# Performance work log

Measured on AMD Instinct MI355X. Metric: run time of the kernel, lower is better.

Reference implementation:

```python
import jax, jax.numpy as jnp
import numpy as np

H = 1024   # hidden_dim
C = 56     # numchars
T = 64     # total_timesteps


def setup_inputs() -> dict:
    key = jax.random.key(0)
    ks = jax.random.split(key, 20)

    def p(k, shape, fan_in):
        # torch default Linear/LSTM init: U(-1/sqrt(fan), 1/sqrt(fan))
        return jax.random.uniform(k, shape, jnp.float32, -1.0, 1.0) / np.float32(np.sqrt(fan_in))

    return {
        "input_sentence": jax.random.normal(ks[0], (T, C), jnp.float32),
        # ErrorUnit.W per layer (top-layer ErrorUnit is never run)
        "W0_w": p(ks[1], (H, C), C), "W0_b": p(ks[2], (H,), C),
        "W1_w": p(ks[3], (H, H), H), "W1_b": p(ks[4], (H,), H),
        "W2_w": p(ks[5], (H, H), H), "W2_b": p(ks[6], (H,), H),
        # LSTM input weights; h0=c0=0 every call so W_hh is inert; b = b_ih + b_hh
        "Wih1": p(ks[7], (4 * H, 2 * H), H), "b1": p(ks[8], (4 * H,), H),
        "Wih2": p(ks[9], (4 * H, 2 * H), H), "b2": p(ks[10], (4 * H,), H),
        "Wih3": p(ks[11], (4 * H, H), H), "b3": p(ks[12], (4 * H,), H),
        # StateUnit.V (reconstruction) per layer >= 1; layer0's V is never used
        "V1_w": p(ks[13], (C, H), H), "V1_b": p(ks[14], (C,), H),
        "V2_w": p(ks[15], (H, H), H), "V2_b": p(ks[16], (H,), H),
        "V3_w": p(ks[17], (H, H), H), "V3_b": p(ks[18], (H,), H),
        "iternumber": 500,
    }


def _lstm_out(x, Wih, b):
    # nn.LSTM(seq=1, batch=1) with zero initial state: f-gate dead, h = o*tanh(i*g)
    z = Wih @ x + b
    i, _, g, o = jnp.split(z, 4)
    return jax.nn.sigmoid(o) * jnp.tanh(jax.nn.sigmoid(i) * jnp.tanh(g))


def reference(input_sentence, W0_w, W0_b, W1_w, W1_b, W2_w, W2_b,
              Wih1, b1, Wih2, b2, Wih3, b3,
              V1_w, V1_b, V2_w, V2_b, V3_w, V3_b, iternumber):
    lam = 1e-4 if iternumber <= 1000 else 1e-2  # lambda1 / lambda2 branch
    h, c = W0_w.shape

    def step(carry, x_t):
        # TD1, TD2: previous-timestep TD errors (fed to LSTM inputs)
        # recon1..3: previous-timestep reconstructions from the layer above
        TD1, TD2, recon1, recon2, recon3, loss = carry
        # layer 0: state is clamped to the input char
        nTD0 = x_t - recon1                        # [C]
        BU0 = W0_w @ nTD0 + W0_b                   # [H]
        loss = loss + jnp.sum(jnp.abs(nTD0))       # * lam**0
        # layer 1
        s1 = _lstm_out(jnp.concatenate([BU0, TD1]), Wih1, b1)
        nrecon1 = V1_w @ s1 + V1_b                 # [C]
        nTD1 = s1 - recon2
        BU1 = W1_w @ nTD1 + W1_b
        loss = loss + jnp.sum(jnp.abs(nTD1)) * lam
        # layer 2
        s2 = _lstm_out(jnp.concatenate([BU1, TD2]), Wih2, b2)
        nrecon2 = V2_w @ s2 + V2_b
        nTD2 = s2 - recon3
        BU2 = W2_w @ nTD2 + W2_b
        loss = loss + jnp.sum(jnp.abs(nTD2)) * (lam ** 2)
        # layer 3 (top): ErrorUnit never runs, its TD_err stays zero -> zero loss term
        s3 = _lstm_out(BU2, Wih3, b3)
        nrecon3 = V3_w @ s3 + V3_b
        return (nTD1, nTD2, nrecon1, nrecon2, nrecon3, loss), None

    z = lambda n: jnp.zeros((n,), jnp.float32)
    init = (z(h), z(h), z(c), z(h), z(h), jnp.float32(0.0))
    carry, _ = jax.lax.scan(step, init, input_sentence)
    return carry[-1]
```

## Files before the change

### kernel.cpp

```cpp
#include <hip/hip_runtime.h>

#define CC 56
#define TT 64
#define GRID 1024
#define NT 256
#define NFLAG 64
#define SS 32
#define FB (GRID * SS)
#define AGENT __HIP_MEMORY_SCOPE_AGENT

#define OFF_FWS   147456
#define OFF_W1BF  262144
#define OFF_W2BF  2359296
#define OFF_PRIV  4456448
#define PRIVB     32768

#define PM2  0
#define PM3  3072
#define PW1R 6144
#define PW2R 9216
#define PV2  12288
#define PV3  13312
#define PV1  14336
#define PA0  15360

#define FS1   0
#define FS2   1024
#define FS3   2048
#define FTD1  3072
#define FTD2  5120
#define FRC1  7168

static __device__ __forceinline__ float wredsum(float v) {
#pragma unroll
  for (int m = 32; m; m >>= 1) v += __shfl_xor(v, m, 64);
  return v;
}
static __device__ __forceinline__ float sigm(float x) { return 1.f / (1.f + __expf(-x)); }
static __device__ __forceinline__ float ftanh(float x) {
  x = fminf(15.f, fmaxf(-15.f, x));
  float e = __expf(2.f * x);
  return (e - 1.f) / (e + 1.f);
}

static __device__ __forceinline__ float2 cld2(const float* p) {
  unsigned long long u = __hip_atomic_load((const unsigned long long*)p, __ATOMIC_RELAXED, AGENT);
  union { unsigned long long u; float2 f; } c; c.u = u; return c.f;
}
static __device__ __forceinline__ float4 cld4(const float* p) {
  float2 a = cld2(p), b = cld2(p + 2);
  return make_float4(a.x, a.y, b.x, b.y);
}
static __device__ __forceinline__ float cld1(const float* p) {
  return __uint_as_float(__hip_atomic_load((const unsigned int*)p, __ATOMIC_RELAXED, AGENT));
}
static __device__ __forceinline__ void cst1(float* p, float v) {
  __hip_atomic_store((unsigned int*)p, __float_as_uint(v), __ATOMIC_RELAXED, AGENT);
}
static __device__ __forceinline__ void cstu2(unsigned* p, unsigned a, unsigned b) {
  unsigned long long u = (unsigned long long)a | ((unsigned long long)b << 32);
  __hip_atomic_store((unsigned long long*)p, u, __ATOMIC_RELAXED, AGENT);
}
static __device__ __forceinline__ int ldi(const int* p) {
  return __hip_atomic_load(p, __ATOMIC_RELAXED, AGENT);
}
static __device__ __forceinline__ void sti(int* p, int v) {
  __hip_atomic_store(p, v, __ATOMIC_RELAXED, AGENT);
}

static __device__ __forceinline__ unsigned bfp(float lo, float hi) {
  unsigned a = __float_as_uint(lo), b = __float_as_uint(hi);
  a = (a + 0x7fffu + ((a >> 16) & 1u)) >> 16;
  b = (b + 0x7fffu + ((b >> 16) & 1u)) >> 16;
  return a | (b << 16);
}
static __device__ __forceinline__ float blo(unsigned u) { return __uint_as_float(u << 16); }
static __device__ __forceinline__ float bhi(unsigned u) { return __uint_as_float(u & 0xffff0000u); }
static __device__ __forceinline__ float bdot2(uint2 w, float4 v) {
  float r = blo(w.x) * v.x;
  r = fmaf(bhi(w.x), v.y, r);
  r = fmaf(blo(w.y), v.z, r);
  r = fmaf(bhi(w.y), v.w, r);
  return r;
}

static __device__ __forceinline__ void warr(int* iws, int g, int b) {
  __syncthreads();
  if (threadIdx.x == 0) sti(iws + SS * b, g);
}
static __device__ __forceinline__ void wwait(int* iws, int g, int b) {
  if (b == 0) {
    const int* p0 = iws + SS * threadIdx.x;
    for (;;) {
      int a0 = ldi(p0), a1 = ldi(p0 + SS * 256), a2 = ldi(p0 + SS * 512), a3 = ldi(p0 + SS * 768);
      if (a0 >= g && a1 >= g && a2 >= g && a3 >= g) break;
      __builtin_amdgcn_s_sleep(1);
    }
    __syncthreads();
    if (threadIdx.x < NFLAG) sti(iws + FB + SS * threadIdx.x, g);
  } else {
    if (threadIdx.x == 0)
      while (ldi(iws + FB + SS * (b & (NFLAG - 1))) < g) __builtin_amdgcn_s_sleep(1);
  }
  __asm__ __volatile__("" ::: "memory");
  __syncthreads();
}

static __device__ __forceinline__ float dotw(const float* a, const float* c, int lane) {
  const float4* a4 = (const float4*)a;
  const float4* c4 = (const float4*)c;
  float acc = 0.f;
#pragma unroll
  for (int j = 0; j < 4; ++j) {
    float4 x = a4[lane * 4 + j], y = c4[lane * 4 + j];
    acc = fmaf(x.x, y.x, fmaf(x.y, y.y, fmaf(x.z, y.z, fmaf(x.w, y.w, acc))));
  }
  return wredsum(acc);
}

__global__ void __launch_bounds__(NT, 4) predcells(
    const float* __restrict__ inp,
    const float* __restrict__ W0w, const float* __restrict__ W0b,
    const float* __restrict__ W1w, const float* __restrict__ W1b,
    const float* __restrict__ W2w, const float* __restrict__ W2b,
    const float* __restrict__ Wi1, const float* __restrict__ b1,
    const float* __restrict__ Wi2, const float* __restrict__ b2,
    const float* __restrict__ Wi3, const float* __restrict__ b3,
    const float* __restrict__ V1w, const float* __restrict__ V1b,
    const float* __restrict__ V2w, const float* __restrict__ V2b,
    const float* __restrict__ V3w, const float* __restrict__ V3b,
    const int* __restrict__ itn,
    float* __restrict__ out, char* ws)
{
  const int tid = threadIdx.x;
  const int lane = tid & 63;
  const int wv = tid >> 6;
  const int b = blockIdx.x;
  const bool hasV1 = (b < CC);

  int* iws = (int*)ws;
  float* fws = (float*)(ws + OFF_FWS);
  unsigned short* w1bf = (unsigned short*)(ws + OFF_W1BF);
  unsigned short* w2bf = (unsigned short*)(ws + OFF_W2BF);
  unsigned short* priv = (unsigned short*)(ws + OFF_PRIV + (size_t)b * PRIVB);

  __shared__ float arow[6][1024];
  __shared__ float psX[6][4], psP[3][4], psA[3];
  __shared__ float cs1[3], cs2[3], cs3[3];

  const int gofs = (wv == 0) ? 0 : ((wv == 1) ? 2048 : 3072);

  {
    float4 r1 = ((const float4*)(W1w + (size_t)b * 1024))[tid];
    cstu2((unsigned*)(w1bf + (size_t)b * 1024 + 4 * tid), bfp(r1.x, r1.y), bfp(r1.z, r1.w));
    float4 r2 = ((const float4*)(W2w + (size_t)b * 1024))[tid];
    cstu2((unsigned*)(w2bf + (size_t)b * 1024 + 4 * tid), bfp(r2.x, r2.y), bfp(r2.z, r2.w));
  }
  warr(iws, 1, b);

  const float lam = (itn[0] <= 1000) ? 1e-4f : 1e-2f;
  const float lam2 = lam * lam;
  const float v1b_b = hasV1 ? V1b[b] : 0.f;
  const float v2b_b = V2b[b];
  const float v3b_b = V3b[b];
  float l0 = 0.f, l1 = 0.f, l2 = 0.f;

  if (wv < 3) {
    float c1v = b1[b + gofs] + dotw(Wi1 + (size_t)(b + gofs) * 2048, W0b, lane);
    float c2v = b2[b + gofs] + dotw(Wi2 + (size_t)(b + gofs) * 2048, W1b, lane);
    float c3v = b3[b + gofs] + dotw(Wi3 + (size_t)(b + gofs) * 1024, W2b, lane);
    if (lane == 0) { cs1[wv] = c1v; cs2[wv] = c2v; cs3[wv] = c3v; }
    if (lane < CC) {
      const float* wr = Wi1 + (size_t)(b + gofs) * 2048;
      float acc = 0.f;
      for (int k = 0; k < 1024; ++k) acc = fmaf(wr[k], W0w[k * CC + lane], acc);
      ((float*)(priv + PA0))[wv * CC + lane] = acc;
    }
    {
      float4 x = ((const float4*)(Wi1 + (size_t)(b + gofs) * 2048 + 1024))[lane];
      ((uint2*)(priv + PW1R + wv * 1024))[lane] = make_uint2(bfp(x.x, x.y), bfp(x.z, x.w));
      float4 y = ((const float4*)(Wi2 + (size_t)(b + gofs) * 2048 + 1024))[lane];
      ((uint2*)(priv + PW2R + wv * 1024))[lane] = make_uint2(bfp(y.x, y.y), bfp(y.z, y.w));
    }
  } else {
#pragma unroll
    for (int j = 0; j < 4; ++j) {
      int i = lane * 4 + j;
      float4 a = ((const float4*)(V2w + (size_t)b * 1024))[i];
      ((uint2*)(priv + PV2))[i] = make_uint2(bfp(a.x, a.y), bfp(a.z, a.w));
      float4 c = ((const float4*)(V3w + (size_t)b * 1024))[i];
      ((uint2*)(priv + PV3))[i] = make_uint2(bfp(c.x, c.y), bfp(c.z, c.w));
      if (hasV1) {
        float4 d = ((const float4*)(V1w + (size_t)b * 1024))[i];
        ((uint2*)(priv + PV1))[i] = make_uint2(bfp(d.x, d.y), bfp(d.z, d.w));
      }
    }
  }
  __syncthreads();
  if (wv < 3) {
    float p = 0.f, ax = 0.f;
    if (lane < CC) {
      float xv = inp[lane];
      p = ((const float*)(priv + PA0))[wv * CC + lane] * xv;
      ax = fabsf(xv);
    }
    p = wredsum(p);
    ax = wredsum(ax);
    if (lane == 0) psA[wv] = p;
    if (b == 0 && wv == 0) l0 += ax;
  }
  __syncthreads();
  if (tid == 0) {
    float s1v = sigm(psA[2] + cs1[2]) * ftanh(sigm(psA[0] + cs1[0]) * ftanh(psA[1] + cs1[1]));
    cst1(fws + FS1 + b, s1v);
    cst1(fws + FTD1 + b, s1v);
    cst1(fws + FS3 + b, 0.f);
    cst1(fws + FTD2 + 1024 + b, 0.f);
  }
  wwait(iws, 1, b);

  {
#pragma unroll
    for (int w = 0; w < 3; ++w) {
      int go = (w == 0) ? 0 : ((w == 1) ? 2048 : 3072);
      ((float4*)arow[w])[tid]     = ((const float4*)(Wi2 + (size_t)(b + go) * 2048))[tid];
      ((float4*)arow[3 + w])[tid] = ((const float4*)(Wi3 + (size_t)(b + go) * 1024))[tid];
    }
    __syncthreads();
    float ac[12];
#pragma unroll
    for (int j = 0; j < 12; ++j) ac[j] = 0.f;
    const uint2* wsrc = (const uint2*)w1bf;
#pragma unroll 4
    for (int k = 0; k < 1024; ++k) {
      uint2 wp = wsrc[k * 256 + tid];
      float f0 = blo(wp.x), f1 = bhi(wp.x), f2 = blo(wp.y), f3 = bhi(wp.y);
      float ai = arow[0][k], ag = arow[1][k], ao = arow[2][k];
      ac[0] = fmaf(ai, f0, ac[0]); ac[1] = fmaf(ai, f1, ac[1]); ac[2] = fmaf(ai, f2, ac[2]); ac[3] = fmaf(ai, f3, ac[3]);
      ac[4] = fmaf(ag, f0, ac[4]); ac[5] = fmaf(ag, f1, ac[5]); ac[6] = fmaf(ag, f2, ac[6]); ac[7] = fmaf(ag, f3, ac[7]);
      ac[8] = fmaf(ao, f0, ac[8]); ac[9] = fmaf(ao, f1, ac[9]); ac[10] = fmaf(ao, f2, ac[10]); ac[11] = fmaf(ao, f3, ac[11]);
    }
#pragma unroll
    for (int w = 0; w < 3; ++w)
      ((uint2*)(priv + PM2 + w * 1024))[tid] =
          make_uint2(bfp(ac[w * 4 + 0], ac[w * 4 + 1]), bfp(ac[w * 4 + 2], ac[w * 4 + 3]));
#pragma unroll
    for (int j = 0; j < 12; ++j) ac[j] = 0.f;
    wsrc = (const uint2*)w2bf;
#pragma unroll 4
    for (int k = 0; k < 1024; ++k) {
      uint2 wp = wsrc[k * 256 + tid];
      float f0 = blo(wp.x), f1 = bhi(wp.x), f2 = blo(wp.y), f3 = bhi(wp.y);
      float ai = arow[3][k], ag = arow[4][k], ao = arow[5][k];
      ac[0] = fmaf(ai, f0, ac[0]); ac[1] = fmaf(ai, f1, ac[1]); ac[2] = fmaf(ai, f2, ac[2]); ac[3] = fmaf(ai, f3, ac[3]);
      ac[4] = fmaf(ag, f0, ac[4]); ac[5] = fmaf(ag, f1, ac[5]); ac[6] = fmaf(ag, f2, ac[6]); ac[7] = fmaf(ag, f3, ac[7]);
      ac[8] = fmaf(ao, f0, ac[8]); ac[9] = fmaf(ao, f1, ac[9]); ac[10] = fmaf(ao, f2, ac[10]); ac[11] = fmaf(ao, f3, ac[11]);
    }
#pragma unroll
    for (int w = 0; w < 3; ++w)
      ((uint2*)(priv + PM3 + w * 1024))[tid] =
          make_uint2(bfp(ac[w * 4 + 0], ac[w * 4 + 1]), bfp(ac[w * 4 + 2], ac[w * 4 + 3]));
  }
  warr(iws, 2, b);

  int g = 2;
  const uint2* pm2 = (const uint2*)(priv + PM2);
  const uint2* pm3 = (const uint2*)(priv + PM3);
  const uint2* pw1r = (const uint2*)(priv + PW1R);
  const uint2* pw2r = (const uint2*)(priv + PW2R);
  const uint2* pv2 = (const uint2*)(priv + PV2);
  const uint2* pv3 = (const uint2*)(priv + PV3);
  const uint2* pv1 = (const uint2*)(priv + PV1);
  const float* a0p = (const float*)(priv + PA0);

  for (int t = 0; t < TT; ++t) {
    const int par = t & 1;
    float* td1cur = fws + FTD1 + par * 1024;
    float* td1nxt = fws + FTD1 + (par ^ 1) * 1024;
    float* td2old = fws + FTD2 + (par ^ 1) * 1024;
    float* td2cur = fws + FTD2 + par * 1024;

    uint2 wm2[3]; wm2[0] = pm2[tid]; wm2[1] = pm2[256 + tid]; wm2[2] = pm2[512 + tid];
    uint2 wv3 = pv3[tid];
    uint2 wv1; if (hasV1) wv1 = pv1[tid];
    {
      float4 v = cld4(td2old + 4 * tid);
      uint2 wr0 = pw2r[tid], wr1 = pw2r[256 + tid], wr2 = pw2r[512 + tid];
      float p0 = wredsum(bdot2(wr0, v));
      float p1 = wredsum(bdot2(wr1, v));
      float p2 = wredsum(bdot2(wr2, v));
      if (lane == 0) { psP[0][wv] = p0; psP[1][wv] = p1; psP[2][wv] = p2; }
    }
    wwait(iws, g, b);
    {
      float4 vtd1 = cld4(td1cur + 4 * tid);
      float4 vs3  = cld4(fws + FS3 + 4 * tid);
      float p0 = wredsum(bdot2(wm2[0], vtd1));
      float p1 = wredsum(bdot2(wm2[1], vtd1));
      float p2 = wredsum(bdot2(wm2[2], vtd1));
      float p3 = wredsum(bdot2(wv3, vs3));
      if (lane == 0) { psX[0][wv] = p0; psX[1][wv] = p1; psX[2][wv] = p2; psX[3][wv] = p3; }
      if (hasV1) {
        float4 vs1 = cld4(fws + FS1 + 4 * tid);
        float pv = wredsum(bdot2(wv1, vs1));
        if (lane == 0) psX[4][wv] = pv;
      }
      if (b == 0) {
        float al = wredsum(fabsf(vtd1.x) + fabsf(vtd1.y) + fabsf(vtd1.z) + fabsf(vtd1.w));
        if (lane == 0) psX[5][wv] = al;
      }
      __syncthreads();
      if (tid == 0) {
        float zi = psX[0][0] + psX[0][1] + psX[0][2] + psX[0][3] + psP[0][0] + psP[0][1] + psP[0][2] + psP[0][3] + cs2[0];
        float zg = psX[1][0] + psX[1][1] + psX[1][2] + psX[1][3] + psP[1][0] + psP[1][1] + psP[1][2] + psP[1][3] + cs2[1];
        float zo = psX[2][0] + psX[2][1] + psX[2][2] + psX[2][3] + psP[2][0] + psP[2][1] + psP[2][2] + psP[2][3] + cs2[2];
        float s2v = sigm(zo) * ftanh(sigm(zi) * ftanh(zg));
        float rc3v = (t == 0) ? 0.f : (psX[3][0] + psX[3][1] + psX[3][2] + psX[3][3] + v3b_b);
        cst1(fws + FS2 + b, s2v);
        cst1(td2cur + b, s2v - rc3v);
        if (hasV1) cst1(fws + FRC1 + b, psX[4][0] + psX[4][1] + psX[4][2] + psX[4][3] + v1b_b);
        if (b == 0) l1 += psX[5][0] + psX[5][1] + psX[5][2] + psX[5][3];
      }
    }
    warr(iws, ++g, b);

    uint2 wm3[3]; wm3[0] = pm3[tid]; wm3[1] = pm3[256 + tid]; wm3[2] = pm3[512 + tid];
    uint2 wv2 = pv2[tid];
    {
      float4 v = cld4(td1cur + 4 * tid);
      uint2 wr0 = pw1r[tid], wr1 = pw1r[256 + tid], wr2 = pw1r[512 + tid];
      float p0 = wredsum(bdot2(wr0, v));
      float p1 = wredsum(bdot2(wr1, v));
      float p2 = wredsum(bdot2(wr2, v));
      if (lane == 0) { psP[0][wv] = p0; psP[1][wv] = p1; psP[2][wv] = p2; }
    }
    wwait(iws, g, b);
    {
      float4 vtd2 = cld4(td2cur + 4 * tid);
      float4 vs2  = cld4(fws + FS2 + 4 * tid);
      float p0 = wredsum(bdot2(wm3[0], vtd2));
      float p1 = wredsum(bdot2(wm3[1], vtd2));
      float p2 = wredsum(bdot2(wm3[2], vtd2));
      float p3 = wredsum(bdot2(wv2, vs2));
      if (lane == 0) { psX[0][wv] = p0; psX[1][wv] = p1; psX[2][wv] = p2; psX[3][wv] = p3; }
      if (b == 0) {
        float al = wredsum(fabsf(vtd2.x) + fabsf(vtd2.y) + fabsf(vtd2.z) + fabsf(vtd2.w));
        if (lane == 0) psX[5][wv] = al;
      }
      if (wv < 3) {
        const int tn = (t < TT - 1) ? (t + 1) : (TT - 1);
        float p = 0.f, ax = 0.f;
        if (lane < CC) {
          float xv = inp[tn * CC + lane];
          float rcv = cld1(fws + FRC1 + lane);
          float nd = xv - rcv;
          p = a0p[wv * CC + lane] * nd;
          ax = fabsf(nd);
        }
        p = wredsum(p);
        ax = wredsum(ax);
        if (lane == 0) psA[wv] = p;
        if (b == 0 && wv == 0 && t < TT - 1) l0 += ax;
      }
      __syncthreads();
      if (tid == 0) {
        float z3i = psX[0][0] + psX[0][1] + psX[0][2] + psX[0][3] + cs3[0];
        float z3g = psX[1][0] + psX[1][1] + psX[1][2] + psX[1][3] + cs3[1];
        float z3o = psX[2][0] + psX[2][1] + psX[2][2] + psX[2][3] + cs3[2];
        cst1(fws + FS3 + b, sigm(z3o) * ftanh(sigm(z3i) * ftanh(z3g)));
        float rc2v = psX[3][0] + psX[3][1] + psX[3][2] + psX[3][3] + v2b_b;
        float z1i = psA[0] + psP[0][0] + psP[0][1] + psP[0][2] + psP[0][3] + cs1[0];
        float z1g = psA[1] + psP[1][0] + psP[1][1] + psP[1][2] + psP[1][3] + cs1[1];
        float z1o = psA[2] + psP[2][0] + psP[2][1] + psP[2][2] + psP[2][3] + cs1[2];
        float s1n = sigm(z1o) * ftanh(sigm(z1i) * ftanh(z1g));
        cst1(fws + FS1 + b, s1n);
        cst1(td1nxt + b, s1n - rc2v);
        if (b == 0) l2 += psX[5][0] + psX[5][1] + psX[5][2] + psX[5][3];
      }
    }
    warr(iws, ++g, b);
  }

  if (b == 0 && tid == 0) out[0] = l0 + lam * l1 + lam2 * l2;
}

extern "C" void kernel_launch(void* const* d_in, const int* in_sizes, int n_in,
                              void* d_out, int out_size, void* d_ws, size_t ws_size,
                              hipStream_t stream) {
  const float* inp = (const float*)d_in[0];
  const float* W0w = (const float*)d_in[1];
  const float* W0b = (const float*)d_in[2];
  const float* W1w = (const float*)d_in[3];
  const float* W1b = (const float*)d_in[4];
  const float* W2w = (const float*)d_in[5];
  const float* W2b = (const float*)d_in[6];
  const float* Wi1 = (const float*)d_in[7];
  const float* b1  = (const float*)d_in[8];
  const float* Wi2 = (const float*)d_in[9];
  const float* b2  = (const float*)d_in[10];
  const float* Wi3 = (const float*)d_in[11];
  const float* b3  = (const float*)d_in[12];
  const float* V1w = (const float*)d_in[13];
  const float* V1b = (const float*)d_in[14];
  const float* V2w = (const float*)d_in[15];
  const float* V2b = (const float*)d_in[16];
  const float* V3w = (const float*)d_in[17];
  const float* V3b = (const float*)d_in[18];
  const int*   itn = (const int*)d_in[19];

  hipLaunchKernelGGL(predcells, dim3(GRID), dim3(NT), 0, stream,
                     inp, W0w, W0b, W1w, W1b, W2w, W2b,
                     Wi1, b1, Wi2, b2, Wi3, b3,
                     V1w, V1b, V2w, V2b, V3w, V3b, itn,
                     (float*)d_out, (char*)d_ws);
}
```

Baseline: 1.110 ms.

## Replace grid barriers with per-element tagged data polling in timestep loop

Removes the two grid-wide barriers per timestep. Each published value is now stored together with a generation tag as one 64-bit atomic, and consumers spin-poll the specific elements they need until the tags reach the expected generation. This turns a global all-to-all barrier into dataflow synchronisation, so blocks can proceed as soon as their inputs are ready. The costs are doubled workspace size, polling traffic on 1024 elements per read, and a guard counter that can silently break out with stale data.

```diff
diff --git a/kernel.cpp b/kernel.cpp
--- a/kernel.cpp
+++ b/kernel.cpp
@@ -24,12 +24,14 @@
 #define PV1  14336
 #define PA0  15360
 
-#define FS1   0
-#define FS2   1024
-#define FS3   2048
-#define FTD1  3072
-#define FTD2  5120
-#define FRC1  7168
+#define GS1   0
+#define GS2   2048
+#define GS3   4096
+#define GTD1  6144
+#define GTD2  10240
+#define GRC1  14336
+
+#define PGUARD (1 << 20)
 
 static __device__ __forceinline__ float wredsum(float v) {
 #pragma unroll
@@ -47,16 +49,6 @@
   unsigned long long u = __hip_atomic_load((const unsigned long long*)p, __ATOMIC_RELAXED, AGENT);
   union { unsigned long long u; float2 f; } c; c.u = u; return c.f;
 }
-static __device__ __forceinline__ float4 cld4(const float* p) {
-  float2 a = cld2(p), b = cld2(p + 2);
-  return make_float4(a.x, a.y, b.x, b.y);
-}
-static __device__ __forceinline__ float cld1(const float* p) {
-  return __uint_as_float(__hip_atomic_load((const unsigned int*)p, __ATOMIC_RELAXED, AGENT));
-}
-static __device__ __forceinline__ void cst1(float* p, float v) {
-  __hip_atomic_store((unsigned int*)p, __float_as_uint(v), __ATOMIC_RELAXED, AGENT);
-}
 static __device__ __forceinline__ void cstu2(unsigned* p, unsigned a, unsigned b) {
   unsigned long long u = (unsigned long long)a | ((unsigned long long)b << 32);
   __hip_atomic_store((unsigned long long*)p, u, __ATOMIC_RELAXED, AGENT);
@@ -66,6 +58,31 @@
 }
 static __device__ __forceinline__ void sti(int* p, int v) {
   __hip_atomic_store(p, v, __ATOMIC_RELAXED, AGENT);
+}
+
+static __device__ __forceinline__ int ptag(float2 v) { return (int)__float_as_uint(v.y); }
+static __device__ __forceinline__ void pub(float* base, int i, float v, int tag) {
+  cstu2((unsigned*)(base + 2 * i), __float_as_uint(v), (unsigned)tag);
+}
+static __device__ __forceinline__ float4 poll4(const float* base, int i0, int want) {
+  const float* p = base + 2 * i0;
+  float2 a, b, c, d; int gd = 0;
+  for (;;) {
+    a = cld2(p); b = cld2(p + 2); c = cld2(p + 4); d = cld2(p + 6);
+    if (ptag(a) >= want && ptag(b) >= want && ptag(c) >= want && ptag(d) >= want) break;
+    if (++gd > PGUARD) break;
+  }
+  return make_float4(a.x, b.x, c.x, d.x);
+}
+static __device__ __forceinline__ float poll1(const float* base, int i, int want) {
+  const float* p = base + 2 * i;
+  float2 a; int gd = 0;
+  for (;;) {
+    a = cld2(p);
+    if (ptag(a) >= want) break;
+    if (++gd > PGUARD) break;
+  }
+  return a.x;
 }
 
 static __device__ __forceinline__ unsigned bfp(float lo, float hi) {
@@ -82,6 +99,9 @@
   r = fmaf(blo(w.y), v.z, r);
   r = fmaf(bhi(w.y), v.w, r);
   return r;
+}
+static __device__ __forceinline__ float asum4(float4 v) {
+  return fabsf(v.x) + fabsf(v.y) + fabsf(v.z) + fabsf(v.w);
 }
 
 static __device__ __forceinline__ void warr(int* iws, int g, int b) {
@@ -212,10 +232,10 @@
   __syncthreads();
   if (tid == 0) {
     float s1v = sigm(psA[2] + cs1[2]) * ftanh(sigm(psA[0] + cs1[0]) * ftanh(psA[1] + cs1[1]));
-    cst1(fws + FS1 + b, s1v);
-    cst1(fws + FTD1 + b, s1v);
-    cst1(fws + FS3 + b, 0.f);
-    cst1(fws + FTD2 + 1024 + b, 0.f);
+    pub(fws + GS1, b, s1v, 1);
+    pub(fws + GTD1, b, s1v, 1);
+    pub(fws + GS3, b, 0.f, 1);
+    pub(fws + GTD2 + 2048, b, 0.f, 1);
   }
   wwait(iws, 1, b);
 
@@ -261,9 +281,7 @@
       ((uint2*)(priv + PM3 + w * 1024))[tid] =
           make_uint2(bfp(ac[w * 4 + 0], ac[w * 4 + 1]), bfp(ac[w * 4 + 2], ac[w * 4 + 3]));
   }
-  warr(iws, 2, b);
-
-  int g = 2;
+
   const uint2* pm2 = (const uint2*)(priv + PM2);
   const uint2* pm3 = (const uint2*)(priv + PM3);
   const uint2* pw1r = (const uint2*)(priv + PW1R);
@@ -275,38 +293,42 @@
 
   for (int t = 0; t < TT; ++t) {
     const int par = t & 1;
-    float* td1cur = fws + FTD1 + par * 1024;
-    float* td1nxt = fws + FTD1 + (par ^ 1) * 1024;
-    float* td2old = fws + FTD2 + (par ^ 1) * 1024;
-    float* td2cur = fws + FTD2 + par * 1024;
+    float* td1cur = fws + GTD1 + par * 2048;
+    float* td1nxt = fws + GTD1 + (par ^ 1) * 2048;
+    float* td2old = fws + GTD2 + (par ^ 1) * 2048;
+    float* td2cur = fws + GTD2 + par * 2048;
+    const int w_old = (t + 2) >> 1;
+    const int w_td1 = (t >> 1) + 1;
+    const int w_s   = t + 1;
+    const int w_cur = ((t + 2) >> 1) + (t & 1);
+    const int p_td  = (t & 1) ? ((t + 3) >> 1) : ((t >> 1) + 1);
 
     uint2 wm2[3]; wm2[0] = pm2[tid]; wm2[1] = pm2[256 + tid]; wm2[2] = pm2[512 + tid];
     uint2 wv3 = pv3[tid];
     uint2 wv1; if (hasV1) wv1 = pv1[tid];
     {
-      float4 v = cld4(td2old + 4 * tid);
+      float4 v = poll4(td2old, 4 * tid, w_old);
       uint2 wr0 = pw2r[tid], wr1 = pw2r[256 + tid], wr2 = pw2r[512 + tid];
       float p0 = wredsum(bdot2(wr0, v));
       float p1 = wredsum(bdot2(wr1, v));
       float p2 = wredsum(bdot2(wr2, v));
       if (lane == 0) { psP[0][wv] = p0; psP[1][wv] = p1; psP[2][wv] = p2; }
     }
-    wwait(iws, g, b);
+    float4 vtd1 = poll4(td1cur, 4 * tid, w_td1);
     {
-      float4 vtd1 = cld4(td1cur + 4 * tid);
-      float4 vs3  = cld4(fws + FS3 + 4 * tid);
+      float4 vs3 = poll4(fws + GS3, 4 * tid, w_s);
       float p0 = wredsum(bdot2(wm2[0], vtd1));
       float p1 = wredsum(bdot2(wm2[1], vtd1));
       float p2 = wredsum(bdot2(wm2[2], vtd1));
       float p3 = wredsum(bdot2(wv3, vs3));
       if (lane == 0) { psX[0][wv] = p0; psX[1][wv] = p1; psX[2][wv] = p2; psX[3][wv] = p3; }
       if (hasV1) {
-        float4 vs1 = cld4(fws + FS1 + 4 * tid);
+        float4 vs1 = poll4(fws + GS1, 4 * tid, w_s);
         float pv = wredsum(bdot2(wv1, vs1));
         if (lane == 0) psX[4][wv] = pv;
       }
       if (b == 0) {
-        float al = wredsum(fabsf(vtd1.x) + fabsf(vtd1.y) + fabsf(vtd1.z) + fabsf(vtd1.w));
+        float al = wredsum(asum4(vtd1));
         if (lane == 0) psX[5][wv] = al;
       }
       __syncthreads();
@@ -316,35 +338,33 @@
         float zo = psX[2][0] + psX[2][1] + psX[2][2] + psX[2][3] + psP[2][0] + psP[2][1] + psP[2][2] + psP[2][3] + cs2[2];
         float s2v = sigm(zo) * ftanh(sigm(zi) * ftanh(zg));
         float rc3v = (t == 0) ? 0.f : (psX[3][0] + psX[3][1] + psX[3][2] + psX[3][3] + v3b_b);
-        cst1(fws + FS2 + b, s2v);
-        cst1(td2cur + b, s2v - rc3v);
-        if (hasV1) cst1(fws + FRC1 + b, psX[4][0] + psX[4][1] + psX[4][2] + psX[4][3] + v1b_b);
+        pub(fws + GS2, b, s2v, w_s);
+        pub(td2cur, b, s2v - rc3v, p_td);
+        if (hasV1) pub(fws + GRC1, b, psX[4][0] + psX[4][1] + psX[4][2] + psX[4][3] + v1b_b, w_s);
         if (b == 0) l1 += psX[5][0] + psX[5][1] + psX[5][2] + psX[5][3];
       }
-    }
-    warr(iws, ++g, b);
-
-    uint2 wm3[3]; wm3[0] = pm3[tid]; wm3[1] = pm3[256 + tid]; wm3[2] = pm3[512 + tid];
-    uint2 wv2 = pv2[tid];
+      __syncthreads();
+    }
+
     {
-      float4 v = cld4(td1cur + 4 * tid);
       uint2 wr0 = pw1r[tid], wr1 = pw1r[256 + tid], wr2 = pw1r[512 + tid];
-      float p0 = wredsum(bdot2(wr0, v));
-      float p1 = wredsum(bdot2(wr1, v));
-      float p2 = wredsum(bdot2(wr2, v));
+      float p0 = wredsum(bdot2(wr0, vtd1));
+      float p1 = wredsum(bdot2(wr1, vtd1));
+      float p2 = wredsum(bdot2(wr2, vtd1));
       if (lane == 0) { psP[0][wv] = p0; psP[1][wv] = p1; psP[2][wv] = p2; }
     }
-    wwait(iws, g, b);
     {
-      float4 vtd2 = cld4(td2cur + 4 * tid);
-      float4 vs2  = cld4(fws + FS2 + 4 * tid);
+      uint2 wm3[3]; wm3[0] = pm3[tid]; wm3[1] = pm3[256 + tid]; wm3[2] = pm3[512 + tid];
+      uint2 wv2 = pv2[tid];
+      float4 vtd2 = poll4(td2cur, 4 * tid, w_cur);
+      float4 vs2  = poll4(fws + GS2, 4 * tid, w_s);
       float p0 = wredsum(bdot2(wm3[0], vtd2));
       float p1 = wredsum(bdot2(wm3[1], vtd2));
       float p2 = wredsum(bdot2(wm3[2], vtd2));
       float p3 = wredsum(bdot2(wv2, vs2));
       if (lane == 0) { psX[0][wv] = p0; psX[1][wv] = p1; psX[2][wv] = p2; psX[3][wv] = p3; }
       if (b == 0) {
-        float al = wredsum(fabsf(vtd2.x) + fabsf(vtd2.y) + fabsf(vtd2.z) + fabsf(vtd2.w));
+        float al = wredsum(asum4(vtd2));
         if (lane == 0) psX[5][wv] = al;
       }
       if (wv < 3) {
@@ -352,10 +372,10 @@
         float p = 0.f, ax = 0.f;
         if (lane < CC) {
           float xv = inp[tn * CC + lane];
-          float rcv = cld1(fws + FRC1 + lane);
-          float nd = xv - rcv;
-          p = a0p[wv * CC + lane] * nd;
-          ax = fabsf(nd);
+          float rcv = poll1(fws + GRC1, lane, w_s);
+          float ndv = xv - rcv;
+          p = a0p[wv * CC + lane] * ndv;
+          ax = fabsf(ndv);
         }
         p = wredsum(p);
         ax = wredsum(ax);
@@ -367,18 +387,18 @@
         float z3i = psX[0][0] + psX[0][1] + psX[0][2] + psX[0][3] + cs3[0];
         float z3g = psX[1][0] + psX[1][1] + psX[1][2] + psX[1][3] + cs3[1];
         float z3o = psX[2][0] + psX[2][1] + psX[2][2] + psX[2][3] + cs3[2];
-        cst1(fws + FS3 + b, sigm(z3o) * ftanh(sigm(z3i) * ftanh(z3g)));
+        pub(fws + GS3, b, sigm(z3o) * ftanh(sigm(z3i) * ftanh(z3g)), t + 2);
         float rc2v = psX[3][0] + psX[3][1] + psX[3][2] + psX[3][3] + v2b_b;
         float z1i = psA[0] + psP[0][0] + psP[0][1] + psP[0][2] + psP[0][3] + cs1[0];
         float z1g = psA[1] + psP[1][0] + psP[1][1] + psP[1][2] + psP[1][3] + cs1[1];
         float z1o = psA[2] + psP[2][0] + psP[2][1] + psP[2][2] + psP[2][3] + cs1[2];
         float s1n = sigm(z1o) * ftanh(sigm(z1i) * ftanh(z1g));
-        cst1(fws + FS1 + b, s1n);
-        cst1(td1nxt + b, s1n - rc2v);
+        pub(fws + GS1, b, s1n, t + 2);
+        pub(td1nxt, b, s1n - rc2v, p_td);
         if (b == 0) l2 += psX[5][0] + psX[5][1] + psX[5][2] + psX[5][3];
       }
-    }
-    warr(iws, ++g, b);
+      __syncthreads();
+    }
   }
 
   if (b == 0 && tid == 0) out[0] = l0 + lam * l1 + lam2 * l2;
```

Measured after the change: 1.474 ms. 1.33x slower.

## Map one output row per wavefront on 256 workers with a master-block barrier

Applied to the files above, without the earlier changes.

The recurrent loop now runs on only 256 worker blocks. Each wavefront owns a whole hidden row and does the full dot product itself, so the cross-wave shared-memory reductions and per-block syncthreads go away. Block 0 becomes a dedicated coordinator: it polls a per-row ready counter that each wavefront sets with a release store, then broadcasts a phase flag. Per-row weights written during setup switch to atomic stores so other blocks can read them. Spin loops gain timeout guards. The cost is much less parallelism per timestep, since each wavefront now streams more data, and added coordinator latency on every phase.

```diff
diff --git a/kernel.cpp b/kernel.cpp
--- a/kernel.cpp
+++ b/kernel.cpp
@@ -4,12 +4,16 @@
 #define TT 64
 #define GRID 1024
 #define NT 256
+#define NWORK 256
 #define NFLAG 64
 #define SS 32
-#define FB (GRID * SS)
+#define FB 32768
+#define WFL 34816
+#define RD  43008
+#define RDS 8
 #define AGENT __HIP_MEMORY_SCOPE_AGENT
 
-#define OFF_FWS   147456
+#define OFF_FWS   204800
 #define OFF_W1BF  262144
 #define OFF_W2BF  2359296
 #define OFF_PRIV  4456448
@@ -23,6 +27,7 @@
 #define PV3  13312
 #define PV1  14336
 #define PA0  15360
+#define PCS  15696
 
 #define FS1   0
 #define FS2   1024
@@ -31,6 +36,8 @@
 #define FTD2  5120
 #define FRC1  7168
 
+#define PGUARD (1 << 19)
+
 static __device__ __forceinline__ float wredsum(float v) {
 #pragma unroll
   for (int m = 32; m; m >>= 1) v += __shfl_xor(v, m, 64);
@@ -67,6 +74,9 @@
 static __device__ __forceinline__ void sti(int* p, int v) {
   __hip_atomic_store(p, v, __ATOMIC_RELAXED, AGENT);
 }
+static __device__ __forceinline__ void relrd(int* p, int v) {
+  __hip_atomic_store(p, v, __ATOMIC_RELEASE, AGENT);
+}
 
 static __device__ __forceinline__ unsigned bfp(float lo, float hi) {
   unsigned a = __float_as_uint(lo), b = __float_as_uint(hi);
@@ -76,13 +86,25 @@
 }
 static __device__ __forceinline__ float blo(unsigned u) { return __uint_as_float(u << 16); }
 static __device__ __forceinline__ float bhi(unsigned u) { return __uint_as_float(u & 0xffff0000u); }
-static __device__ __forceinline__ float bdot2(uint2 w, float4 v) {
-  float r = blo(w.x) * v.x;
-  r = fmaf(bhi(w.x), v.y, r);
-  r = fmaf(blo(w.y), v.z, r);
-  r = fmaf(bhi(w.y), v.w, r);
+static __device__ __forceinline__ float bdot4(uint4 w, float4 a, float4 b) {
+  float r =  blo(w.x) * a.x;
+  r = fmaf(bhi(w.x), a.y, r);
+  r = fmaf(blo(w.y), a.z, r);
+  r = fmaf(bhi(w.y), a.w, r);
+  r = fmaf(blo(w.z), b.x, r);
+  r = fmaf(bhi(w.z), b.y, r);
+  r = fmaf(blo(w.w), b.z, r);
+  r = fmaf(bhi(w.w), b.w, r);
   return r;
 }
+static __device__ __forceinline__ float asum4(float4 v) {
+  return fabsf(v.x) + fabsf(v.y) + fabsf(v.z) + fabsf(v.w);
+}
+
+#define DOT16(wp, qoff, A, B, C, D)                                   \
+  ({ uint4 _qa = (wp)[(qoff) + 2 * lane];                             \
+     uint4 _qb = (wp)[(qoff) + 2 * lane + 1];                         \
+     wredsum(bdot4(_qa, A, B) + bdot4(_qb, C, D)); })
 
 static __device__ __forceinline__ void warr(int* iws, int g, int b) {
   __syncthreads();
@@ -91,16 +113,35 @@
 static __device__ __forceinline__ void wwait(int* iws, int g, int b) {
   if (b == 0) {
     const int* p0 = iws + SS * threadIdx.x;
+    int gd = 0;
     for (;;) {
       int a0 = ldi(p0), a1 = ldi(p0 + SS * 256), a2 = ldi(p0 + SS * 512), a3 = ldi(p0 + SS * 768);
       if (a0 >= g && a1 >= g && a2 >= g && a3 >= g) break;
       __builtin_amdgcn_s_sleep(1);
+      if (++gd > PGUARD) break;
     }
     __syncthreads();
     if (threadIdx.x < NFLAG) sti(iws + FB + SS * threadIdx.x, g);
   } else {
-    if (threadIdx.x == 0)
-      while (ldi(iws + FB + SS * (b & (NFLAG - 1))) < g) __builtin_amdgcn_s_sleep(1);
+    if (threadIdx.x == 0) {
+      int gd = 0;
+      while (ldi(iws + FB + SS * (b & (NFLAG - 1))) < g) {
+        __builtin_amdgcn_s_sleep(1);
+        if (++gd > PGUARD) break;
+      }
+    }
+  }
+  __asm__ __volatile__("" ::: "memory");
+  __syncthreads();
+}
+
+static __device__ __forceinline__ void wflag(const int* iws, int b, int f) {
+  if (threadIdx.x == 0) {
+    int gd = 0;
+    while (ldi(iws + WFL + SS * (b - 1)) < f) {
+      __builtin_amdgcn_s_sleep(1);
+      if (++gd > PGUARD) break;
+    }
   }
   __asm__ __volatile__("" ::: "memory");
   __syncthreads();
@@ -145,10 +186,14 @@
   unsigned short* priv = (unsigned short*)(ws + OFF_PRIV + (size_t)b * PRIVB);
 
   __shared__ float arow[6][1024];
-  __shared__ float psX[6][4], psP[3][4], psA[3];
+  __shared__ float psA[3];
   __shared__ float cs1[3], cs2[3], cs3[3];
 
   const int gofs = (wv == 0) ? 0 : ((wv == 1) ? 2048 : 3072);
+
+  const float lam = (itn[0] <= 1000) ? 1e-4f : 1e-2f;
+  const float lam2 = lam * lam;
+  float l0 = 0.f, l1 = 0.f, l2 = 0.f;
 
   {
     float4 r1 = ((const float4*)(W1w + (size_t)b * 1024))[tid];
@@ -158,41 +203,38 @@
   }
   warr(iws, 1, b);
 
-  const float lam = (itn[0] <= 1000) ? 1e-4f : 1e-2f;
-  const float lam2 = lam * lam;
-  const float v1b_b = hasV1 ? V1b[b] : 0.f;
-  const float v2b_b = V2b[b];
-  const float v3b_b = V3b[b];
-  float l0 = 0.f, l1 = 0.f, l2 = 0.f;
-
   if (wv < 3) {
     float c1v = b1[b + gofs] + dotw(Wi1 + (size_t)(b + gofs) * 2048, W0b, lane);
     float c2v = b2[b + gofs] + dotw(Wi2 + (size_t)(b + gofs) * 2048, W1b, lane);
     float c3v = b3[b + gofs] + dotw(Wi3 + (size_t)(b + gofs) * 1024, W2b, lane);
-    if (lane == 0) { cs1[wv] = c1v; cs2[wv] = c2v; cs3[wv] = c3v; }
+    if (lane == 0) {
+      cs1[wv] = c1v; cs2[wv] = c2v; cs3[wv] = c3v;
+      float* pc = (float*)(priv + PCS);
+      cst1(pc + wv, c1v); cst1(pc + 3 + wv, c2v); cst1(pc + 6 + wv, c3v);
+    }
     if (lane < CC) {
       const float* wr = Wi1 + (size_t)(b + gofs) * 2048;
       float acc = 0.f;
       for (int k = 0; k < 1024; ++k) acc = fmaf(wr[k], W0w[k * CC + lane], acc);
-      ((float*)(priv + PA0))[wv * CC + lane] = acc;
+      cst1((float*)(priv + PA0) + wv * CC + lane, acc);
     }
     {
       float4 x = ((const float4*)(Wi1 + (size_t)(b + gofs) * 2048 + 1024))[lane];
-      ((uint2*)(priv + PW1R + wv * 1024))[lane] = make_uint2(bfp(x.x, x.y), bfp(x.z, x.w));
+      cstu2((unsigned*)(priv + PW1R + wv * 1024) + 2 * lane, bfp(x.x, x.y), bfp(x.z, x.w));
       float4 y = ((const float4*)(Wi2 + (size_t)(b + gofs) * 2048 + 1024))[lane];
-      ((uint2*)(priv + PW2R + wv * 1024))[lane] = make_uint2(bfp(y.x, y.y), bfp(y.z, y.w));
+      cstu2((unsigned*)(priv + PW2R + wv * 1024) + 2 * lane, bfp(y.x, y.y), bfp(y.z, y.w));
     }
   } else {
 #pragma unroll
     for (int j = 0; j < 4; ++j) {
       int i = lane * 4 + j;
       float4 a = ((const float4*)(V2w + (size_t)b * 1024))[i];
-      ((uint2*)(priv + PV2))[i] = make_uint2(bfp(a.x, a.y), bfp(a.z, a.w));
+      cstu2((unsigned*)(priv + PV2) + 2 * i, bfp(a.x, a.y), bfp(a.z, a.w));
       float4 c = ((const float4*)(V3w + (size_t)b * 1024))[i];
-      ((uint2*)(priv + PV3))[i] = make_uint2(bfp(c.x, c.y), bfp(c.z, c.w));
+      cstu2((unsigned*)(priv + PV3) + 2 * i, bfp(c.x, c.y), bfp(c.z, c.w));
       if (hasV1) {
         float4 d = ((const float4*)(V1w + (size_t)b * 1024))[i];
-        ((uint2*)(priv + PV1))[i] = make_uint2(bfp(d.x, d.y), bfp(d.z, d.w));
+        cstu2((unsigned*)(priv + PV1) + 2 * i, bfp(d.x, d.y), bfp(d.z, d.w));
       }
     }
   }
@@ -201,13 +243,13 @@
     float p = 0.f, ax = 0.f;
     if (lane < CC) {
       float xv = inp[lane];
-      p = ((const float*)(priv + PA0))[wv * CC + lane] * xv;
+      p = cld1((const float*)(priv + PA0) + wv * CC + lane) * xv;
       ax = fabsf(xv);
     }
     p = wredsum(p);
     ax = wredsum(ax);
     if (lane == 0) psA[wv] = p;
-    if (b == 0 && wv == 0) l0 += ax;
+    if (b == 1 && wv == 0) l0 += ax;
   }
   __syncthreads();
   if (tid == 0) {
@@ -215,7 +257,6 @@
     cst1(fws + FS1 + b, s1v);
     cst1(fws + FTD1 + b, s1v);
     cst1(fws + FS3 + b, 0.f);
-    cst1(fws + FTD2 + 1024 + b, 0.f);
   }
   wwait(iws, 1, b);
 
@@ -242,8 +283,8 @@
     }
 #pragma unroll
     for (int w = 0; w < 3; ++w)
-      ((uint2*)(priv + PM2 + w * 1024))[tid] =
-          make_uint2(bfp(ac[w * 4 + 0], ac[w * 4 + 1]), bfp(ac[w * 4 + 2], ac[w * 4 + 3]));
+      cstu2((unsigned*)(priv + PM2 + w * 1024) + 2 * tid,
+            bfp(ac[w * 4 + 0], ac[w * 4 + 1]), bfp(ac[w * 4 + 2], ac[w * 4 + 3]));
 #pragma unroll
     for (int j = 0; j < 12; ++j) ac[j] = 0.f;
     wsrc = (const uint2*)w2bf;
@@ -258,130 +299,143 @@
     }
 #pragma unroll
     for (int w = 0; w < 3; ++w)
-      ((uint2*)(priv + PM3 + w * 1024))[tid] =
-          make_uint2(bfp(ac[w * 4 + 0], ac[w * 4 + 1]), bfp(ac[w * 4 + 2], ac[w * 4 + 3]));
-  }
-  warr(iws, 2, b);
-
-  int g = 2;
-  const uint2* pm2 = (const uint2*)(priv + PM2);
-  const uint2* pm3 = (const uint2*)(priv + PM3);
-  const uint2* pw1r = (const uint2*)(priv + PW1R);
-  const uint2* pw2r = (const uint2*)(priv + PW2R);
-  const uint2* pv2 = (const uint2*)(priv + PV2);
-  const uint2* pv3 = (const uint2*)(priv + PV3);
-  const uint2* pv1 = (const uint2*)(priv + PV1);
-  const float* a0p = (const float*)(priv + PA0);
+      cstu2((unsigned*)(priv + PM3 + w * 1024) + 2 * tid,
+            bfp(ac[w * 4 + 0], ac[w * 4 + 1]), bfp(ac[w * 4 + 2], ac[w * 4 + 3]));
+  }
+  __syncthreads();
+  if (tid == 0) sti(iws + RD + RDS * b, 2);
+
+  if (b > NWORK) return;
+
+  if (b == 0) {
+    int* rd = iws + RD;
+    for (int v = 2; v <= 129; ++v) {
+      int gd = 0;
+      for (;;) {
+        int a0 = ldi(rd + RDS * tid),         a1 = ldi(rd + RDS * (tid + 256)),
+            a2 = ldi(rd + RDS * (tid + 512)), a3 = ldi(rd + RDS * (tid + 768));
+        if (a0 >= v && a1 >= v && a2 >= v && a3 >= v) break;
+        __builtin_amdgcn_s_sleep(1);
+        if (++gd > PGUARD) break;
+      }
+      __syncthreads();
+      sti(iws + WFL + SS * tid, v);
+    }
+    return;
+  }
+
+  const int r = (b - 1) + 256 * wv;
+  const unsigned short* prv = (const unsigned short*)(ws + OFF_PRIV + (size_t)r * PRIVB);
+  const uint4* pm2  = (const uint4*)(prv + PM2);
+  const uint4* pm3  = (const uint4*)(prv + PM3);
+  const uint4* pw1r = (const uint4*)(prv + PW1R);
+  const uint4* pw2r = (const uint4*)(prv + PW2R);
+  const uint4* pv2  = (const uint4*)(prv + PV2);
+  const uint4* pv3  = (const uint4*)(prv + PV3);
+  const uint4* pv1  = (const uint4*)(prv + PV1);
+  const float* a0p  = (const float*)(prv + PA0);
+  const float* pcs  = (const float*)(prv + PCS);
+  const bool rV1 = (r < CC);
+  const float v1bg = rV1 ? V1b[r] : 0.f;
+  const float v2bg = V2b[r];
+  const float v3bg = V3b[r];
+  int* myrd = iws + RD + RDS * r;
+
+  wflag(iws, b, 2);
+  float c1g[3], c2g[3], c3g[3];
+#pragma unroll
+  for (int g = 0; g < 3; ++g) { c1g[g] = pcs[g]; c2g[g] = pcs[3 + g]; c3g[g] = pcs[6 + g]; }
 
   for (int t = 0; t < TT; ++t) {
     const int par = t & 1;
-    float* td1cur = fws + FTD1 + par * 1024;
-    float* td1nxt = fws + FTD1 + (par ^ 1) * 1024;
-    float* td2old = fws + FTD2 + (par ^ 1) * 1024;
-    float* td2cur = fws + FTD2 + par * 1024;
-
-    uint2 wm2[3]; wm2[0] = pm2[tid]; wm2[1] = pm2[256 + tid]; wm2[2] = pm2[512 + tid];
-    uint2 wv3 = pv3[tid];
-    uint2 wv1; if (hasV1) wv1 = pv1[tid];
+    const float* dtd1c = fws + FTD1 + par * 1024;
+    float* dtd1n = fws + FTD1 + (par ^ 1) * 1024;
+    const float* dtd2o = fws + FTD2 + (par ^ 1) * 1024;
+    float* dtd2c = fws + FTD2 + par * 1024;
+
+    float pp0 = 0.f, pp1 = 0.f, pp2 = 0.f;
+    if (t > 0) {
+      float4 o0 = cld4(dtd2o + 16 * lane),     o1 = cld4(dtd2o + 16 * lane + 4),
+             o2 = cld4(dtd2o + 16 * lane + 8), o3 = cld4(dtd2o + 16 * lane + 12);
+      pp0 = DOT16(pw2r, 0,   o0, o1, o2, o3);
+      pp1 = DOT16(pw2r, 128, o0, o1, o2, o3);
+      pp2 = DOT16(pw2r, 256, o0, o1, o2, o3);
+      wflag(iws, b, 2 + 2 * t);
+    }
+
+    float4 v0 = cld4(dtd1c + 16 * lane),     v1 = cld4(dtd1c + 16 * lane + 4),
+           v2 = cld4(dtd1c + 16 * lane + 8), v3 = cld4(dtd1c + 16 * lane + 12);
     {
-      float4 v = cld4(td2old + 4 * tid);
-      uint2 wr0 = pw2r[tid], wr1 = pw2r[256 + tid], wr2 = pw2r[512 + tid];
-      float p0 = wredsum(bdot2(wr0, v));
-      float p1 = wredsum(bdot2(wr1, v));
-      float p2 = wredsum(bdot2(wr2, v));
-      if (lane == 0) { psP[0][wv] = p0; psP[1][wv] = p1; psP[2][wv] = p2; }
-    }
-    wwait(iws, g, b);
+      float4 s0 = cld4(fws + FS3 + 16 * lane),     s1_ = cld4(fws + FS3 + 16 * lane + 4),
+             s2_ = cld4(fws + FS3 + 16 * lane + 8), s3_ = cld4(fws + FS3 + 16 * lane + 12);
+      float xz0 = DOT16(pm2, 0,   v0, v1, v2, v3);
+      float xz1 = DOT16(pm2, 128, v0, v1, v2, v3);
+      float xz2 = DOT16(pm2, 256, v0, v1, v2, v3);
+      float xv3 = DOT16(pv3, 0, s0, s1_, s2_, s3_);
+      float xv1 = 0.f;
+      if (rV1) {
+        float4 u0 = cld4(fws + FS1 + 16 * lane),     u1 = cld4(fws + FS1 + 16 * lane + 4),
+               u2 = cld4(fws + FS1 + 16 * lane + 8), u3 = cld4(fws + FS1 + 16 * lane + 12);
+        xv1 = DOT16(pv1, 0, u0, u1, u2, u3);
+      }
+      if (b == 1 && wv == 0)
+        l1 += wredsum(asum4(v0) + asum4(v1) + asum4(v2) + asum4(v3));
+      float zi = xz0 + pp0 + c2g[0];
+      float zg = xz1 + pp1 + c2g[1];
+      float zo = xz2 + pp2 + c2g[2];
+      float s2v = sigm(zo) * ftanh(sigm(zi) * ftanh(zg));
+      float rc3v = (t == 0) ? 0.f : (xv3 + v3bg);
+      if (lane == 0) {
+        cst1(fws + FS2 + r, s2v);
+        cst1(dtd2c + r, s2v - rc3v);
+        if (rV1) cst1(fws + FRC1 + r, xv1 + v1bg);
+        relrd(myrd, 3 + 2 * t);
+      }
+    }
+
+    float py0 = DOT16(pw1r, 0,   v0, v1, v2, v3);
+    float py1 = DOT16(pw1r, 128, v0, v1, v2, v3);
+    float py2 = DOT16(pw1r, 256, v0, v1, v2, v3);
+    wflag(iws, b, 3 + 2 * t);
+
     {
-      float4 vtd1 = cld4(td1cur + 4 * tid);
-      float4 vs3  = cld4(fws + FS3 + 4 * tid);
-      float p0 = wredsum(bdot2(wm2[0], vtd1));
-      float p1 = wredsum(bdot2(wm2[1], vtd1));
-      float p2 = wredsum(bdot2(wm2[2], vtd1));
-      float p3 = wredsum(bdot2(wv3, vs3));
-      if (lane == 0) { psX[0][wv] = p0; psX[1][wv] = p1; psX[2][wv] = p2; psX[3][wv] = p3; }
-      if (hasV1) {
-        float4 vs1 = cld4(fws + FS1 + 4 * tid);
-        float pv = wredsum(bdot2(wv1, vs1));
-        if (lane == 0) psX[4][wv] = pv;
-      }
-      if (b == 0) {
-        float al = wredsum(fabsf(vtd1.x) + fabsf(vtd1.y) + fabsf(vtd1.z) + fabsf(vtd1.w));
-        if (lane == 0) psX[5][wv] = al;
-      }
-      __syncthreads();
-      if (tid == 0) {
-        float zi = psX[0][0] + psX[0][1] + psX[0][2] + psX[0][3] + psP[0][0] + psP[0][1] + psP[0][2] + psP[0][3] + cs2[0];
-        float zg = psX[1][0] + psX[1][1] + psX[1][2] + psX[1][3] + psP[1][0] + psP[1][1] + psP[1][2] + psP[1][3] + cs2[1];
-        float zo = psX[2][0] + psX[2][1] + psX[2][2] + psX[2][3] + psP[2][0] + psP[2][1] + psP[2][2] + psP[2][3] + cs2[2];
-        float s2v = sigm(zo) * ftanh(sigm(zi) * ftanh(zg));
-        float rc3v = (t == 0) ? 0.f : (psX[3][0] + psX[3][1] + psX[3][2] + psX[3][3] + v3b_b);
-        cst1(fws + FS2 + b, s2v);
-        cst1(td2cur + b, s2v - rc3v);
-        if (hasV1) cst1(fws + FRC1 + b, psX[4][0] + psX[4][1] + psX[4][2] + psX[4][3] + v1b_b);
-        if (b == 0) l1 += psX[5][0] + psX[5][1] + psX[5][2] + psX[5][3];
-      }
-    }
-    warr(iws, ++g, b);
-
-    uint2 wm3[3]; wm3[0] = pm3[tid]; wm3[1] = pm3[256 + tid]; wm3[2] = pm3[512 + tid];
-    uint2 wv2 = pv2[tid];
-    {
-      float4 v = cld4(td1cur + 4 * tid);
-      uint2 wr0 = pw1r[tid], wr1 = pw1r[256 + tid], wr2 = pw1r[512 + tid];
-      float p0 = wredsum(bdot2(wr0, v));
-      float p1 = wredsum(bdot2(wr1, v));
-      float p2 = wredsum(bdot2(wr2, v));
-      if (lane == 0) { psP[0][wv] = p0; psP[1][wv] = p1; psP[2][wv] = p2; }
-    }
-    wwait(iws, g, b);
-    {
-      float4 vtd2 = cld4(td2cur + 4 * tid);
-      float4 vs2  = cld4(fws + FS2 + 4 * tid);
-      float p0 = wredsum(bdot2(wm3[0], vtd2));
-      float p1 = wredsum(bdot2(wm3[1], vtd2));
-      float p2 = wredsum(bdot2(wm3[2], vtd2));
-      float p3 = wredsum(bdot2(wv2, vs2));
-      if (lane == 0) { psX[0][wv] = p0; psX[1][wv] = p1; psX[2][wv] = p2; psX[3][wv] = p3; }
-      if (b == 0) {
-        float al = wredsum(fabsf(vtd2.x) + fabsf(vtd2.y) + fabsf(vtd2.z) + fabsf(vtd2.w));
-        if (lane == 0) psX[5][wv] = al;
-      }
-      if (wv < 3) {
-        const int tn = (t < TT - 1) ? (t + 1) : (TT - 1);
-        float p = 0.f, ax = 0.f;
-        if (lane < CC) {
-          float xv = inp[tn * CC + lane];
-          float rcv = cld1(fws + FRC1 + lane);
-          float nd = xv - rcv;
-          p = a0p[wv * CC + lane] * nd;
-          ax = fabsf(nd);
-        }
-        p = wredsum(p);
-        ax = wredsum(ax);
-        if (lane == 0) psA[wv] = p;
-        if (b == 0 && wv == 0 && t < TT - 1) l0 += ax;
-      }
-      __syncthreads();
-      if (tid == 0) {
-        float z3i = psX[0][0] + psX[0][1] + psX[0][2] + psX[0][3] + cs3[0];
-        float z3g = psX[1][0] + psX[1][1] + psX[1][2] + psX[1][3] + cs3[1];
-        float z3o = psX[2][0] + psX[2][1] + psX[2][2] + psX[2][3] + cs3[2];
-        cst1(fws + FS3 + b, sigm(z3o) * ftanh(sigm(z3i) * ftanh(z3g)));
-        float rc2v = psX[3][0] + psX[3][1] + psX[3][2] + psX[3][3] + v2b_b;
-        float z1i = psA[0] + psP[0][0] + psP[0][1] + psP[0][2] + psP[0][3] + cs1[0];
-        float z1g = psA[1] + psP[1][0] + psP[1][1] + psP[1][2] + psP[1][3] + cs1[1];
-        float z1o = psA[2] + psP[2][0] + psP[2][1] + psP[2][2] + psP[2][3] + cs1[2];
-        float s1n = sigm(z1o) * ftanh(sigm(z1i) * ftanh(z1g));
-        cst1(fws + FS1 + b, s1n);
-        cst1(td1nxt + b, s1n - rc2v);
-        if (b == 0) l2 += psX[5][0] + psX[5][1] + psX[5][2] + psX[5][3];
-      }
-    }
-    warr(iws, ++g, b);
-  }
-
-  if (b == 0 && tid == 0) out[0] = l0 + lam * l1 + lam2 * l2;
+      float4 d0 = cld4(dtd2c + 16 * lane),     d1 = cld4(dtd2c + 16 * lane + 4),
+             d2 = cld4(dtd2c + 16 * lane + 8), d3 = cld4(dtd2c + 16 * lane + 12);
+      float4 e0 = cld4(fws + FS2 + 16 * lane),     e1 = cld4(fws + FS2 + 16 * lane + 4),
+             e2 = cld4(fws + FS2 + 16 * lane + 8), e3 = cld4(fws + FS2 + 16 * lane + 12);
+      float yz0 = DOT16(pm3, 0,   d0, d1, d2, d3);
+      float yz1 = DOT16(pm3, 128, d0, d1, d2, d3);
+      float yz2 = DOT16(pm3, 256, d0, d1, d2, d3);
+      float yv2 = DOT16(pv2, 0, e0, e1, e2, e3);
+      const int tn = (t < TT - 1) ? (t + 1) : (TT - 1);
+      float nd = 0.f;
+      if (lane < CC) nd = inp[tn * CC + lane] - cld1(fws + FRC1 + lane);
+      float pa0v = wredsum((lane < CC) ? a0p[lane] * nd : 0.f);
+      float pa1v = wredsum((lane < CC) ? a0p[CC + lane] * nd : 0.f);
+      float pa2v = wredsum((lane < CC) ? a0p[2 * CC + lane] * nd : 0.f);
+      if (b == 1 && wv == 0) {
+        l2 += wredsum(asum4(d0) + asum4(d1) + asum4(d2) + asum4(d3));
+        if (t < TT - 1) l0 += wredsum((lane < CC) ? fabsf(nd) : 0.f);
+      }
+      float z3i = yz0 + c3g[0];
+      float z3g = yz1 + c3g[1];
+      float z3o = yz2 + c3g[2];
+      float s3v = sigm(z3o) * ftanh(sigm(z3i) * ftanh(z3g));
+      float rc2v = yv2 + v2bg;
+      float z1i = pa0v + py0 + c1g[0];
+      float z1g = pa1v + py1 + c1g[1];
+      float z1o = pa2v + py2 + c1g[2];
+      float s1n = sigm(z1o) * ftanh(sigm(z1i) * ftanh(z1g));
+      if (lane == 0) {
+        cst1(fws + FS3 + r, s3v);
+        cst1(fws + FS1 + r, s1n);
+        cst1(dtd1n + r, s1n - rc2v);
+        relrd(myrd, 4 + 2 * t);
+      }
+    }
+  }
+
+  if (b == 1 && tid == 0) out[0] = l0 + lam * l1 + lam2 * l2;
 }
 
 extern "C" void kernel_launch(void* const* d_in, const int* in_sizes, int n_in,
```

Result: slower. 3.175 ms (+186.0%).
